# Kernel tuning notes

Hardware: AMD Instinct MI355X
Metric: run time of the kernel (lower is better)

The kernel has to match this reference:

```python
import jax, jax.numpy as jnp
import numpy as np

B, L, E = 128, 512, 128
NUM_Q, NUM_C, DIFF = 10000, 300, 100


def _lin(k, fan_in, fan_out):
    kw, kb = jax.random.split(k)
    s = 1.0 / np.sqrt(fan_in)
    W = jax.random.uniform(kw, (fan_in, fan_out), jnp.float32, -s, s)
    b = jax.random.uniform(kb, (fan_out,), jnp.float32, -s, s)
    return W, b


def setup_inputs() -> dict:
    key = jax.random.key(0)
    ks = jax.random.split(key, 24)
    inp = {
        "q": jax.random.randint(ks[0], (B, L), 0, NUM_Q),
        "c": jax.random.randint(ks[1], (B, L), 0, NUM_C),
        "sd": jax.random.randint(ks[2], (B, L), 0, DIFF + 99),
        "qd": jax.random.randint(ks[3], (B, L), 0, DIFF + 99),
        "a": jax.random.randint(ks[4], (B, L), 0, 2 * NUM_Q + 1),
        "qshft": jax.random.randint(ks[5], (B, L), 0, NUM_Q),
        "cshft": jax.random.randint(ks[6], (B, L), 0, NUM_C),
        "sdshft": jax.random.randint(ks[7], (B, L), 0, DIFF + 99),
        "qdshft": jax.random.randint(ks[8], (B, L), 0, DIFF + 99),
        "knowledge": jax.random.normal(ks[9], (1, E), jnp.float32) * 0.1,
        "q_tab": jax.random.normal(ks[10], (NUM_Q + 1, E), jnp.float32),
        "c_tab": jax.random.normal(ks[11], (NUM_C + 1, E), jnp.float32),
        "sd_tab": jax.random.normal(ks[12], (DIFF + 100, E), jnp.float32),
        "qd_tab": jax.random.normal(ks[13], (DIFF + 100, E), jnp.float32),
        "a_tab": jax.random.normal(ks[14], (2 * NUM_Q + 2, E), jnp.float32),
    }
    for name, fan_in, ki in [("1", 4 * E, 15), ("2", E, 16), ("3", E, 17),
                             ("4", 2 * E, 18), ("5", 2 * E, 19), ("6", 4 * E, 20)]:
        W, b = _lin(ks[ki], fan_in, E)
        inp[f"W{name}"], inp[f"b{name}"] = W, b
    Wf, bf = _lin(ks[21], E, 10)
    inp["Wf"], inp["bf"] = Wf, bf
    return inp


def reference(q, c, sd, qd, a, qshft, cshft, sdshft, qdshft,
              knowledge, q_tab, c_tab, sd_tab, qd_tab, a_tab,
              W1, b1, W2, b2, W3, b3, W4, b4, W5, b5, W6, b6, Wf, bf):
    # Embedding lookups  [B, L, E]
    q_e, c_e = q_tab[q], c_tab[c]
    sd_e, qd_e = sd_tab[sd], qd_tab[qd]
    a_e = a_tab[a]
    # input_data = linear_1(cat(q,c,sd,qd))  [B, L, E]
    inp = jnp.concatenate([q_e, c_e, sd_e, qd_e], -1) @ W1 + b1
    # (target_data in the torch code is dead: never used for the output)

    k0 = jnp.broadcast_to(knowledge, (q.shape[0], knowledge.shape[1]))  # [B, E]

    def step(k, xs):
        x, sd1, a1, qd1 = xs  # each [B, E]
        qq = x - k
        SDFt = jax.nn.sigmoid(qq @ W2 + b2) * jnp.tanh(qq @ W3 + b3)  # dropout=eval
        xa = jnp.concatenate([SDFt, a1], -1)
        PKAt = jax.nn.sigmoid(xa @ W4 + b4) * jnp.tanh(xa @ W5 + b5)
        ins = jnp.concatenate([k, a1, sd1, qd1], -1)
        gK = jax.nn.sigmoid(ins @ W6 + b6)
        k_new = gK * k + (1.0 - gK) * PKAt
        return k_new, k_new @ Wf + bf

    xs = (jnp.swapaxes(inp, 0, 1), jnp.swapaxes(sd_e, 0, 1),
          jnp.swapaxes(a_e, 0, 1), jnp.swapaxes(qd_e, 0, 1))  # [L, B, E]
    _, logits = jax.lax.scan(step, k0, xs)  # [L, B, 10]
    return jax.nn.sigmoid(jnp.swapaxes(logits, 0, 1))  # [B, L, 10]
```

## Files before the change

kernel.cpp:

```cpp
#include <hip/hip_runtime.h>
#include <hip/hip_bf16.h>
#include <stdint.h>

#define E_DIM 128
#define L_SEQ 512
#define B_SZ  128

typedef _Float16 h2 __attribute__((ext_vector_type(2)));

constexpr size_t SZ_W12 = 512 * 128 * 4;
constexpr size_t SZ_TQ  = 10001 * 128 * 4;
constexpr size_t SZ_TC  = 301 * 128 * 4;
constexpr size_t SZ_TS  = 200 * 128 * 4;
constexpr size_t SZ_TA  = 20002 * 128 * 4;
constexpr size_t SZ_K   = (size_t)B_SZ * L_SEQ * 128 * 4;

constexpr size_t OFF_W12  = 0;
constexpr size_t OFF_W13  = OFF_W12 + SZ_W12;
constexpr size_t OFF_BV2  = OFF_W13 + SZ_W12;
constexpr size_t OFF_BV3  = OFF_BV2 + 512;
constexpr size_t OFF_TQ2  = OFF_BV3 + 512;
constexpr size_t OFF_TQ3  = OFF_TQ2 + SZ_TQ;
constexpr size_t OFF_TC2  = OFF_TQ3 + SZ_TQ;
constexpr size_t OFF_TC3  = OFF_TC2 + SZ_TC;
constexpr size_t OFF_TSD2 = OFF_TC3 + SZ_TC;
constexpr size_t OFF_TSD3 = OFF_TSD2 + SZ_TS;
constexpr size_t OFF_TSD6 = OFF_TSD3 + SZ_TS;
constexpr size_t OFF_TQD2 = OFF_TSD6 + SZ_TS;
constexpr size_t OFF_TQD3 = OFF_TQD2 + SZ_TS;
constexpr size_t OFF_TQD6 = OFF_TQD3 + SZ_TS;
constexpr size_t OFF_TA4  = OFF_TQD6 + SZ_TS;
constexpr size_t OFF_TA5  = OFF_TA4 + SZ_TA;
constexpr size_t OFF_TA6  = OFF_TA5 + SZ_TA;
constexpr size_t OFF_K    = OFF_TA6 + SZ_TA;

__device__ __forceinline__ float fdot2f(unsigned int a, unsigned int b, float c) {
#if __has_builtin(__builtin_amdgcn_fdot2)
  return __builtin_amdgcn_fdot2(__builtin_bit_cast(h2, a), __builtin_bit_cast(h2, b), c, false);
#else
  h2 x = __builtin_bit_cast(h2, a), y = __builtin_bit_cast(h2, b);
  return c + (float)x[0] * (float)y[0] + (float)x[1] * (float)y[1];
#endif
}

__device__ __forceinline__ unsigned int packh2(float a, float b) {
  h2 v; v[0] = (_Float16)a; v[1] = (_Float16)b;
  return __builtin_bit_cast(unsigned int, v);
}

__device__ __forceinline__ float fsig(float x) {
  float t = __builtin_amdgcn_exp2f(-1.4426950408889634f * x);
  return __builtin_amdgcn_rcpf(1.0f + t);
}
__device__ __forceinline__ float ftanh(float x) {
  float t = __builtin_amdgcn_exp2f(2.8853900817779268f * x);
  return 1.0f - 2.0f * __builtin_amdgcn_rcpf(t + 1.0f);
}

#define BARRIER_RAW() asm volatile("s_waitcnt lgkmcnt(0)\n\ts_barrier" ::: "memory")

__global__ __launch_bounds__(128, 1) void prepA_kernel(
    const float* __restrict__ W1, const float* __restrict__ W2, const float* __restrict__ W3,
    const float* __restrict__ b1, const float* __restrict__ b2, const float* __restrict__ b3,
    char* __restrict__ ws) {
  float* W12 = (float*)(ws + OFF_W12);
  float* W13 = (float*)(ws + OFF_W13);
  float* bv2 = (float*)(ws + OFF_BV2);
  float* bv3 = (float*)(ws + OFF_BV3);
  __shared__ __align__(16) float rowb[8][128];
  const int j = threadIdx.x;
  const int blk = blockIdx.x;
  if (blk < 8) {
    const float* M = (blk < 4) ? W2 : W3;
    float* dst = (blk < 4) ? W12 : W13;
    const int r0 = (blk & 3) * 128;
    float Mcol[128];
#pragma unroll
    for (int t = 0; t < 128; t++) Mcol[t] = M[t * 128 + j];
    for (int rb = 0; rb < 128; rb += 8) {
#pragma unroll
      for (int rr = 0; rr < 8; rr++) rowb[rr][j] = W1[(r0 + rb + rr) * 128 + j];
      __syncthreads();
#pragma unroll
      for (int rr = 0; rr < 8; rr++) {
        float acc = 0.0f;
        const float4* r4 = (const float4*)rowb[rr];
#pragma unroll
        for (int t4 = 0; t4 < 32; t4++) {
          float4 v = r4[t4];
          acc += v.x * Mcol[4 * t4 + 0];
          acc += v.y * Mcol[4 * t4 + 1];
          acc += v.z * Mcol[4 * t4 + 2];
          acc += v.w * Mcol[4 * t4 + 3];
        }
        dst[(r0 + rb + rr) * 128 + j] = acc;
      }
      __syncthreads();
    }
  } else {
    rowb[0][j] = b1[j];
    __syncthreads();
    float a2 = b2[j], a3 = b3[j];
    for (int t = 0; t < 128; t++) {
      float bb = rowb[0][t];
      a2 += bb * W2[t * 128 + j];
      a3 += bb * W3[t * 128 + j];
    }
    bv2[j] = a2;
    bv3[j] = a3;
  }
}

__global__ __launch_bounds__(128, 1) void prepB_kernel(
    const float* __restrict__ q_tab, const float* __restrict__ c_tab,
    const float* __restrict__ sd_tab, const float* __restrict__ qd_tab,
    const float* __restrict__ a_tab,
    const float* __restrict__ W4, const float* __restrict__ W5, const float* __restrict__ W6,
    const float* __restrict__ b4, const float* __restrict__ b5, const float* __restrict__ b6,
    char* __restrict__ ws) {
  const float* W12 = (const float*)(ws + OFF_W12);
  const float* W13 = (const float*)(ws + OFF_W13);
  const float* bv2 = (const float*)(ws + OFF_BV2);
  const float* bv3 = (const float*)(ws + OFF_BV3);

  const float* src = nullptr; const float* M = nullptr; const float* bias = nullptr;
  float* dst = nullptr; int rows = 0;
  switch (blockIdx.y) {
    case 0:  src = q_tab;  rows = 10001; M = W12;             bias = bv2; dst = (float*)(ws + OFF_TQ2);  break;
    case 1:  src = q_tab;  rows = 10001; M = W13;             bias = bv3; dst = (float*)(ws + OFF_TQ3);  break;
    case 2:  src = c_tab;  rows = 301;   M = W12 + 128 * 128; bias = nullptr; dst = (float*)(ws + OFF_TC2);  break;
    case 3:  src = c_tab;  rows = 301;   M = W13 + 128 * 128; bias = nullptr; dst = (float*)(ws + OFF_TC3);  break;
    case 4:  src = sd_tab; rows = 200;   M = W12 + 256 * 128; bias = nullptr; dst = (float*)(ws + OFF_TSD2); break;
    case 5:  src = sd_tab; rows = 200;   M = W13 + 256 * 128; bias = nullptr; dst = (float*)(ws + OFF_TSD3); break;
    case 6:  src = sd_tab; rows = 200;   M = W6  + 256 * 128; bias = nullptr; dst = (float*)(ws + OFF_TSD6); break;
    case 7:  src = qd_tab; rows = 200;   M = W12 + 384 * 128; bias = nullptr; dst = (float*)(ws + OFF_TQD2); break;
    case 8:  src = qd_tab; rows = 200;   M = W13 + 384 * 128; bias = nullptr; dst = (float*)(ws + OFF_TQD3); break;
    case 9:  src = qd_tab; rows = 200;   M = W6  + 384 * 128; bias = nullptr; dst = (float*)(ws + OFF_TQD6); break;
    case 10: src = a_tab;  rows = 20002; M = W4  + 128 * 128; bias = b4;  dst = (float*)(ws + OFF_TA4);  break;
    case 11: src = a_tab;  rows = 20002; M = W5  + 128 * 128; bias = b5;  dst = (float*)(ws + OFF_TA5);  break;
    default: src = a_tab;  rows = 20002; M = W6  + 128 * 128; bias = b6;  dst = (float*)(ws + OFF_TA6);  break;
  }
  const int row0 = blockIdx.x * 128;
  if (row0 >= rows) return;
  const int j = threadIdx.x;
  float Mcol[128];
#pragma unroll
  for (int t = 0; t < 128; t++) Mcol[t] = M[t * 128 + j];
  const float bj = bias ? bias[j] : 0.0f;
  __shared__ __align__(16) float rowb[8][128];
  const int rend = (row0 + 128 < rows) ? (row0 + 128) : rows;
  for (int rb = row0; rb < rend; rb += 8) {
    const int nr = (rb + 8 <= rend) ? 8 : (rend - rb);
#pragma unroll
    for (int rr = 0; rr < 8; rr++)
      rowb[rr][j] = src[(rb + (rr < nr ? rr : 0)) * 128 + j];
    __syncthreads();
#pragma unroll
    for (int rr = 0; rr < 8; rr++) {
      if (rr < nr) {
        float acc = bj;
        const float4* r4 = (const float4*)rowb[rr];
#pragma unroll
        for (int t4 = 0; t4 < 32; t4++) {
          float4 v = r4[t4];
          acc += v.x * Mcol[4 * t4 + 0];
          acc += v.y * Mcol[4 * t4 + 1];
          acc += v.z * Mcol[4 * t4 + 2];
          acc += v.w * Mcol[4 * t4 + 3];
        }
        dst[(rb + rr) * 128 + j] = acc;
      }
    }
    __syncthreads();
  }
}


#define PREFETCH(S, P) do {                                                   \
    int _s = (S);                                                             \
    int _qi = idxb[0][_s], _ci = idxb[1][_s], _si = idxb[2][_s];              \
    int _di = idxb[3][_s], _ai = idxb[4][_s];                                 \
    P##q2 = Tq2[_qi * 128 + j]; P##q3 = Tq3[_qi * 128 + j];                   \
    P##c2 = Tc2[_ci * 128 + j]; P##c3 = Tc3[_ci * 128 + j];                   \
    P##s2 = Ts2[_si * 128 + j]; P##s3 = Ts3[_si * 128 + j];                   \
    P##s6 = Ts6[_si * 128 + j];                                               \
    P##d2 = Td2[_di * 128 + j]; P##d3 = Td3[_di * 128 + j];                   \
    P##d6 = Td6[_di * 128 + j];                                               \
    P##a4 = Ta4[_ai * 128 + j]; P##a5 = Ta5[_ai * 128 + j];                   \
    P##a6 = Ta6[_ai * 128 + j];                                               \
  } while (0)

#define SCAN_STEP(P, S2, L) do {                                              \
                                           \
    float u2a = 0.f, u2b = 0.f, u3a = 0.f, u3b = 0.f, u6a = 0.f, u6b = 0.f;   \
    {                                                                         \
      const uint4* kp4 = ((const uint4*)kpair) + 8 * h;                       \
      _Pragma("unroll")                                                       \
      for (int i = 0; i < 8; i++) {                                           \
        uint4 kv = kp4[i];                                                    \
        u2a = fdot2f(kv.x, w2h[4 * i + 0], u2a);                              \
        u3a = fdot2f(kv.x, w3h[4 * i + 0], u3a);                              \
        u6a = fdot2f(kv.x, w6h[4 * i + 0], u6a);                              \
        u2b = fdot2f(kv.y, w2h[4 * i + 1], u2b);                              \
        u3b = fdot2f(kv.y, w3h[4 * i + 1], u3b);                              \
        u6b = fdot2f(kv.y, w6h[4 * i + 1], u6b);                              \
        u2a = fdot2f(kv.z, w2h[4 * i + 2], u2a);                              \
        u3a = fdot2f(kv.z, w3h[4 * i + 2], u3a);                              \
        u6a = fdot2f(kv.z, w6h[4 * i + 2], u6a);                              \
        u2b = fdot2f(kv.w, w2h[4 * i + 3], u2b);                              \
        u3b = fdot2f(kv.w, w3h[4 * i + 3], u3b);                              \
        u6b = fdot2f(kv.w, w6h[4 * i + 3], u6b);                              \
      }                                                                       \
    }                                                                         \
    pA[0][tid] = u2a + u2b; pA[1][tid] = u3a + u3b; pA[2][tid] = u6a + u6b;   \
    BARRIER_RAW();                                                    \
    float o2 = pA[0][tid ^ 128], o3 = pA[1][tid ^ 128], o6 = pA[2][tid ^ 128];\
    float U2 = (P##q2 + P##c2 + P##s2 + P##d2) - (u2a + u2b + o2);            \
    float U3 = (P##q3 + P##c3 + P##s3 + P##d3) - (u3a + u3b + o3);            \
    float U6 = (P##a6 + P##s6 + P##d6) + (u6a + u6b + o6);                    \
    float sdft = fsig(U2) * ftanh(U3);                                        \
    float g = fsig(U6);                                                       \
    if (!h) ((_Float16*)sdfp)[j] = (_Float16)sdft;                            \
    BARRIER_RAW();                                                    \
                                           \
    float u4a = 0.f, u4b = 0.f, u5a = 0.f, u5b = 0.f;                         \
    {                                                                         \
      const uint4* sp4 = ((const uint4*)sdfp) + 8 * h;                        \
      _Pragma("unroll")                                                       \
      for (int i = 0; i < 8; i++) {                                           \
        uint4 sv = sp4[i];                                                    \
        u4a = fdot2f(sv.x, w4h[4 * i + 0], u4a);                              \
        u5a = fdot2f(sv.x, w5h[4 * i + 0], u5a);                              \
        u4b = fdot2f(sv.y, w4h[4 * i + 1], u4b);                              \
        u5b = fdot2f(sv.y, w5h[4 * i + 1], u5b);                              \
        u4a = fdot2f(sv.z, w4h[4 * i + 2], u4a);                              \
        u5a = fdot2f(sv.z, w5h[4 * i + 2], u5a);                              \
        u4b = fdot2f(sv.w, w4h[4 * i + 3], u4b);                              \
        u5b = fdot2f(sv.w, w5h[4 * i + 3], u5b);                              \
      }                                                                       \
    }                                                                         \
    pB[0][tid] = u4a + u4b; pB[1][tid] = u5a + u5b;                           \
    BARRIER_RAW();                                                    \
    float o4 = pB[0][tid ^ 128], o5 = pB[1][tid ^ 128];                       \
    float pk = fsig(u4a + u4b + o4 + P##a4) * ftanh(u5a + u5b + o5 + P##a5);  \
    k = g * k + (1.0f - g) * pk;                                              \
    if (h) ((_Float16*)kpair)[j] = (_Float16)k;                               \
    BARRIER_RAW();                                                    \
    if (!h) Kout[((size_t)(base + (L))) * 128 + j] = k;                       \
    PREFETCH(S2, P);                                                          \
  } while (0)

__global__ __launch_bounds__(256, 1) void scan_kernel(
    const int* __restrict__ q, const int* __restrict__ c, const int* __restrict__ sd,
    const int* __restrict__ qd, const int* __restrict__ a,
    const float* __restrict__ knowledge,
    const float* __restrict__ W2, const float* __restrict__ W3, const float* __restrict__ W4,
    const float* __restrict__ W5, const float* __restrict__ W6,
    char* __restrict__ ws) {
  const int tid = threadIdx.x;
  const int j = tid & 127;
  const int h = tid >> 7;
  const int b = blockIdx.x;
  const int base = b * L_SEQ;

  const float* Tq2 = (const float*)(ws + OFF_TQ2);
  const float* Tq3 = (const float*)(ws + OFF_TQ3);
  const float* Tc2 = (const float*)(ws + OFF_TC2);
  const float* Tc3 = (const float*)(ws + OFF_TC3);
  const float* Ts2 = (const float*)(ws + OFF_TSD2);
  const float* Ts3 = (const float*)(ws + OFF_TSD3);
  const float* Ts6 = (const float*)(ws + OFF_TSD6);
  const float* Td2 = (const float*)(ws + OFF_TQD2);
  const float* Td3 = (const float*)(ws + OFF_TQD3);
  const float* Td6 = (const float*)(ws + OFF_TQD6);
  const float* Ta4 = (const float*)(ws + OFF_TA4);
  const float* Ta5 = (const float*)(ws + OFF_TA5);
  const float* Ta6 = (const float*)(ws + OFF_TA6);
  float* Kout = (float*)(ws + OFF_K);

  __shared__ int idxb[5][L_SEQ];
  __shared__ __align__(16) unsigned int kpair[64];
  __shared__ __align__(16) unsigned int sdfp[64];
  __shared__ float pA[3][256];
  __shared__ float pB[2][256];

  idxb[0][tid] = q[base + tid];  idxb[0][tid + 256] = q[base + tid + 256];
  idxb[1][tid] = c[base + tid];  idxb[1][tid + 256] = c[base + tid + 256];
  idxb[2][tid] = sd[base + tid]; idxb[2][tid + 256] = sd[base + tid + 256];
  idxb[3][tid] = qd[base + tid]; idxb[3][tid + 256] = qd[base + tid + 256];
  idxb[4][tid] = a[base + tid];  idxb[4][tid + 256] = a[base + tid + 256];

  unsigned int w2h[32], w3h[32], w6h[32], w4h[32], w5h[32];
  const int t0 = h * 64;
#pragma unroll
  for (int p = 0; p < 32; p++) {
    w2h[p] = packh2(W2[(t0 + 2 * p) * 128 + j], W2[(t0 + 2 * p + 1) * 128 + j]);
    w3h[p] = packh2(W3[(t0 + 2 * p) * 128 + j], W3[(t0 + 2 * p + 1) * 128 + j]);
    w6h[p] = packh2(W6[(t0 + 2 * p) * 128 + j], W6[(t0 + 2 * p + 1) * 128 + j]);
    w4h[p] = packh2(W4[(t0 + 2 * p) * 128 + j], W4[(t0 + 2 * p + 1) * 128 + j]);
    w5h[p] = packh2(W5[(t0 + 2 * p) * 128 + j], W5[(t0 + 2 * p + 1) * 128 + j]);
  }

  float k = knowledge[j];
  if (h) ((_Float16*)kpair)[j] = (_Float16)k;
  __syncthreads();

  float gAq2, gAq3, gAc2, gAc3, gAs2, gAs3, gAs6, gAd2, gAd3, gAd6, gAa4, gAa5, gAa6;
  float gBq2, gBq3, gBc2, gBc3, gBs2, gBs3, gBs6, gBd2, gBd3, gBd6, gBa4, gBa5, gBa6;
  PREFETCH(0, gA);
  PREFETCH(1, gB);

#pragma unroll 1
  for (int m = 0; m < L_SEQ / 2; m++) {
    const int l0 = 2 * m;
    const int s2 = (l0 + 2 < L_SEQ) ? (l0 + 2) : (L_SEQ - 1);
    const int s3 = (l0 + 3 < L_SEQ) ? (l0 + 3) : (L_SEQ - 1);
    SCAN_STEP(gA, s2, l0);
    SCAN_STEP(gB, s3, l0 + 1);
  }
}

__global__ __launch_bounds__(256, 4) void logits_kernel(
    const float* __restrict__ Wf, const float* __restrict__ bf,
    const char* __restrict__ ws, float* __restrict__ out) {
  const float* K = (const float*)(ws + OFF_K);
  const int t = blockIdx.x * 256 + threadIdx.x;
  if (t >= B_SZ * L_SEQ * 10) return;
  const int r = t / 10;
  const int i = t - 10 * r;
  float acc = bf[i];
  const float* kr = K + (size_t)r * 128;
#pragma unroll 8
  for (int jj = 0; jj < 128; jj++) acc += kr[jj] * Wf[jj * 10 + i];
  out[t] = fsig(acc);
}

extern "C" void kernel_launch(void* const* d_in, const int* in_sizes, int n_in,
                              void* d_out, int out_size, void* d_ws, size_t ws_size,
                              hipStream_t stream) {
  const int* q  = (const int*)d_in[0];
  const int* c  = (const int*)d_in[1];
  const int* sd = (const int*)d_in[2];
  const int* qd = (const int*)d_in[3];
  const int* a  = (const int*)d_in[4];
  const float* knowledge = (const float*)d_in[9];
  const float* q_tab  = (const float*)d_in[10];
  const float* c_tab  = (const float*)d_in[11];
  const float* sd_tab = (const float*)d_in[12];
  const float* qd_tab = (const float*)d_in[13];
  const float* a_tab  = (const float*)d_in[14];
  const float* W1 = (const float*)d_in[15];
  const float* b1 = (const float*)d_in[16];
  const float* W2 = (const float*)d_in[17];
  const float* b2 = (const float*)d_in[18];
  const float* W3 = (const float*)d_in[19];
  const float* b3 = (const float*)d_in[20];
  const float* W4 = (const float*)d_in[21];
  const float* b4 = (const float*)d_in[22];
  const float* W5 = (const float*)d_in[23];
  const float* b5 = (const float*)d_in[24];
  const float* W6 = (const float*)d_in[25];
  const float* b6 = (const float*)d_in[26];
  const float* Wf = (const float*)d_in[27];
  const float* bf = (const float*)d_in[28];
  char* ws = (char*)d_ws;
  float* out = (float*)d_out;

  prepA_kernel<<<9, 128, 0, stream>>>(W1, W2, W3, b1, b2, b3, ws);
  prepB_kernel<<<dim3(157, 13), 128, 0, stream>>>(q_tab, c_tab, sd_tab, qd_tab, a_tab,
                                                  W4, W5, W6, b4, b5, b6, ws);
  scan_kernel<<<B_SZ, 256, 0, stream>>>(q, c, sd, qd, a, knowledge, W2, W3, W4, W5, W6, ws);
  logits_kernel<<<(B_SZ * L_SEQ * 10 + 255) / 256, 256, 0, stream>>>(Wf, bf, ws, out);
}
```

Before: 924.5 us.

## Use MFMA for table pre-projection, shuffle-based scan reduction, row-wise logits

Replaces the scalar FP32 table-projection kernel with two fp16 MFMA GEMM kernels that project each embedding table through several weight slices at once. The scan kernel is remapped so that the two half-dot-product partners sit in the same wavefront, which turns two LDS exchange barriers per step into lane shuffles, and one barrier moves after the prefetch. The logits kernel now computes all 10 outputs per row from shared-memory weights using float4 loads. This lowers prep and scan overhead but rounds the precomputed tables to fp16 inputs, so accuracy may suffer.

```diff
diff --git a/kernel.cpp b/kernel.cpp
--- a/kernel.cpp
+++ b/kernel.cpp
@@ -7,13 +7,14 @@
 #define B_SZ  128
 
 typedef _Float16 h2 __attribute__((ext_vector_type(2)));
+typedef _Float16 f16x8 __attribute__((ext_vector_type(8)));
+typedef float f32x4 __attribute__((ext_vector_type(4)));
 
 constexpr size_t SZ_W12 = 512 * 128 * 4;
 constexpr size_t SZ_TQ  = 10001 * 128 * 4;
 constexpr size_t SZ_TC  = 301 * 128 * 4;
 constexpr size_t SZ_TS  = 200 * 128 * 4;
 constexpr size_t SZ_TA  = 20002 * 128 * 4;
-constexpr size_t SZ_K   = (size_t)B_SZ * L_SEQ * 128 * 4;
 
 constexpr size_t OFF_W12  = 0;
 constexpr size_t OFF_W13  = OFF_W12 + SZ_W12;
@@ -111,65 +112,136 @@
   }
 }
 
-__global__ __launch_bounds__(128, 1) void prepB_kernel(
+template <int NSEG>
+__global__ __launch_bounds__(256, 1) void gemm_tabs_kernel(
     const float* __restrict__ q_tab, const float* __restrict__ c_tab,
     const float* __restrict__ sd_tab, const float* __restrict__ qd_tab,
     const float* __restrict__ a_tab,
     const float* __restrict__ W4, const float* __restrict__ W5, const float* __restrict__ W6,
     const float* __restrict__ b4, const float* __restrict__ b5, const float* __restrict__ b6,
     char* __restrict__ ws) {
+  constexpr int WD  = NSEG * 128;
+  constexpr int SPAN = WD / 4;
+  constexpr int NCT = SPAN / 16;
+
+  __shared__ _Float16 BT[WD][136];
+  __shared__ _Float16 At[32][136];
+  __shared__ float biasL[384];
+
   const float* W12 = (const float*)(ws + OFF_W12);
   const float* W13 = (const float*)(ws + OFF_W13);
   const float* bv2 = (const float*)(ws + OFF_BV2);
   const float* bv3 = (const float*)(ws + OFF_BV3);
 
-  const float* src = nullptr; const float* M = nullptr; const float* bias = nullptr;
-  float* dst = nullptr; int rows = 0;
-  switch (blockIdx.y) {
-    case 0:  src = q_tab;  rows = 10001; M = W12;             bias = bv2; dst = (float*)(ws + OFF_TQ2);  break;
-    case 1:  src = q_tab;  rows = 10001; M = W13;             bias = bv3; dst = (float*)(ws + OFF_TQ3);  break;
-    case 2:  src = c_tab;  rows = 301;   M = W12 + 128 * 128; bias = nullptr; dst = (float*)(ws + OFF_TC2);  break;
-    case 3:  src = c_tab;  rows = 301;   M = W13 + 128 * 128; bias = nullptr; dst = (float*)(ws + OFF_TC3);  break;
-    case 4:  src = sd_tab; rows = 200;   M = W12 + 256 * 128; bias = nullptr; dst = (float*)(ws + OFF_TSD2); break;
-    case 5:  src = sd_tab; rows = 200;   M = W13 + 256 * 128; bias = nullptr; dst = (float*)(ws + OFF_TSD3); break;
-    case 6:  src = sd_tab; rows = 200;   M = W6  + 256 * 128; bias = nullptr; dst = (float*)(ws + OFF_TSD6); break;
-    case 7:  src = qd_tab; rows = 200;   M = W12 + 384 * 128; bias = nullptr; dst = (float*)(ws + OFF_TQD2); break;
-    case 8:  src = qd_tab; rows = 200;   M = W13 + 384 * 128; bias = nullptr; dst = (float*)(ws + OFF_TQD3); break;
-    case 9:  src = qd_tab; rows = 200;   M = W6  + 384 * 128; bias = nullptr; dst = (float*)(ws + OFF_TQD6); break;
-    case 10: src = a_tab;  rows = 20002; M = W4  + 128 * 128; bias = b4;  dst = (float*)(ws + OFF_TA4);  break;
-    case 11: src = a_tab;  rows = 20002; M = W5  + 128 * 128; bias = b5;  dst = (float*)(ws + OFF_TA5);  break;
-    default: src = a_tab;  rows = 20002; M = W6  + 128 * 128; bias = b6;  dst = (float*)(ws + OFF_TA6);  break;
-  }
-  const int row0 = blockIdx.x * 128;
-  if (row0 >= rows) return;
-  const int j = threadIdx.x;
-  float Mcol[128];
-#pragma unroll
-  for (int t = 0; t < 128; t++) Mcol[t] = M[t * 128 + j];
-  const float bj = bias ? bias[j] : 0.0f;
-  __shared__ __align__(16) float rowb[8][128];
-  const int rend = (row0 + 128 < rows) ? (row0 + 128) : rows;
-  for (int rb = row0; rb < rend; rb += 8) {
-    const int nr = (rb + 8 <= rend) ? 8 : (rend - rb);
-#pragma unroll
-    for (int rr = 0; rr < 8; rr++)
-      rowb[rr][j] = src[(rb + (rr < nr ? rr : 0)) * 128 + j];
+  const int bid = blockIdx.x;
+  const int tid = threadIdx.x;
+  const int wv = tid >> 6, ln = tid & 63;
+
+  const float* src; int rows; int blk_in;
+  const float* bsrc[3]; int koff[3]; const float* bias[3]; float* dst[3];
+  if (NSEG == 2) {
+    if (bid < 79) { src = q_tab; rows = 10001; blk_in = bid;
+      bsrc[0] = W12; bsrc[1] = W13; koff[0] = koff[1] = 0;
+      bias[0] = bv2; bias[1] = bv3;
+      dst[0] = (float*)(ws + OFF_TQ2); dst[1] = (float*)(ws + OFF_TQ3);
+    } else { src = c_tab; rows = 301; blk_in = bid - 79;
+      bsrc[0] = W12; bsrc[1] = W13; koff[0] = koff[1] = 128;
+      bias[0] = bias[1] = nullptr;
+      dst[0] = (float*)(ws + OFF_TC2); dst[1] = (float*)(ws + OFF_TC3);
+    }
+    bsrc[2] = nullptr; koff[2] = 0; bias[2] = nullptr; dst[2] = nullptr;
+  } else {
+    if (bid < 2) { src = sd_tab; rows = 200; blk_in = bid;
+      bsrc[0] = W12; bsrc[1] = W13; bsrc[2] = W6; koff[0] = koff[1] = koff[2] = 256;
+      bias[0] = bias[1] = bias[2] = nullptr;
+      dst[0] = (float*)(ws + OFF_TSD2); dst[1] = (float*)(ws + OFF_TSD3); dst[2] = (float*)(ws + OFF_TSD6);
+    } else if (bid < 4) { src = qd_tab; rows = 200; blk_in = bid - 2;
+      bsrc[0] = W12; bsrc[1] = W13; bsrc[2] = W6; koff[0] = koff[1] = koff[2] = 384;
+      bias[0] = bias[1] = bias[2] = nullptr;
+      dst[0] = (float*)(ws + OFF_TQD2); dst[1] = (float*)(ws + OFF_TQD3); dst[2] = (float*)(ws + OFF_TQD6);
+    } else { src = a_tab; rows = 20002; blk_in = bid - 4;
+      bsrc[0] = W4; bsrc[1] = W5; bsrc[2] = W6; koff[0] = koff[1] = koff[2] = 128;
+      bias[0] = b4; bias[1] = b5; bias[2] = b6;
+      dst[0] = (float*)(ws + OFF_TA4); dst[1] = (float*)(ws + OFF_TA5); dst[2] = (float*)(ws + OFF_TA6);
+    }
+  }
+
+#pragma unroll
+  for (int s = 0; s < NSEG; s++) {
+    const float* M = bsrc[s] + (size_t)koff[s] * 128;
+    const int jj = tid & 127, kb = tid >> 7;
+    for (int k0 = 0; k0 < 128; k0 += 2) {
+      const int k = k0 + kb;
+      BT[s * 128 + jj][k] = (_Float16)M[k * 128 + jj];
+    }
+    if (tid < 128) biasL[s * 128 + tid] = bias[s] ? bias[s][tid] : 0.0f;
+  }
+  __syncthreads();
+
+  f16x8 bf[NCT][4];
+#pragma unroll
+  for (int ct = 0; ct < NCT; ct++)
+#pragma unroll
+    for (int kt = 0; kt < 4; kt++) {
+      const int col = wv * SPAN + ct * 16 + (ln & 15);
+      const int k = kt * 32 + (ln >> 4) * 8;
+      bf[ct][kt] = *(const f16x8*)&BT[col][k];
+    }
+  float bvl[NCT];
+#pragma unroll
+  for (int ct = 0; ct < NCT; ct++) bvl[ct] = biasL[wv * SPAN + ct * 16 + (ln & 15)];
+
+  const int row_base = blk_in * 128;
+  for (int ch = 0; ch < 4; ch++) {
+    const int row0 = row_base + ch * 32;
+    {
+      const int r = tid >> 3, cb = (tid & 7) * 16;
+      int sr = row0 + r; if (sr >= rows) sr = rows - 1;
+      const float4* s4 = (const float4*)(src + (size_t)sr * 128 + cb);
+      float4 v0 = s4[0], v1 = s4[1], v2 = s4[2], v3 = s4[3];
+      f16x8 lo, hi;
+      lo[0] = (_Float16)v0.x; lo[1] = (_Float16)v0.y; lo[2] = (_Float16)v0.z; lo[3] = (_Float16)v0.w;
+      lo[4] = (_Float16)v1.x; lo[5] = (_Float16)v1.y; lo[6] = (_Float16)v1.z; lo[7] = (_Float16)v1.w;
+      hi[0] = (_Float16)v2.x; hi[1] = (_Float16)v2.y; hi[2] = (_Float16)v2.z; hi[3] = (_Float16)v2.w;
+      hi[4] = (_Float16)v3.x; hi[5] = (_Float16)v3.y; hi[6] = (_Float16)v3.z; hi[7] = (_Float16)v3.w;
+      *(f16x8*)&At[r][cb] = lo;
+      *(f16x8*)&At[r][cb + 8] = hi;
+    }
     __syncthreads();
-#pragma unroll
-    for (int rr = 0; rr < 8; rr++) {
-      if (rr < nr) {
-        float acc = bj;
-        const float4* r4 = (const float4*)rowb[rr];
-#pragma unroll
-        for (int t4 = 0; t4 < 32; t4++) {
-          float4 v = r4[t4];
-          acc += v.x * Mcol[4 * t4 + 0];
-          acc += v.y * Mcol[4 * t4 + 1];
-          acc += v.z * Mcol[4 * t4 + 2];
-          acc += v.w * Mcol[4 * t4 + 3];
+    f16x8 af[2][4];
+#pragma unroll
+    for (int rt = 0; rt < 2; rt++)
+#pragma unroll
+      for (int kt = 0; kt < 4; kt++) {
+        const int row = rt * 16 + (ln & 15);
+        const int k = kt * 32 + (ln >> 4) * 8;
+        af[rt][kt] = *(const f16x8*)&At[row][k];
+      }
+    f32x4 acc[2][NCT];
+#pragma unroll
+    for (int rt = 0; rt < 2; rt++)
+#pragma unroll
+      for (int ct = 0; ct < NCT; ct++) acc[rt][ct] = (f32x4){0.f, 0.f, 0.f, 0.f};
+#pragma unroll
+    for (int kt = 0; kt < 4; kt++)
+#pragma unroll
+      for (int ct = 0; ct < NCT; ct++)
+#pragma unroll
+        for (int rt = 0; rt < 2; rt++)
+          acc[rt][ct] = __builtin_amdgcn_mfma_f32_16x16x32_f16(af[rt][kt], bf[ct][kt], acc[rt][ct], 0, 0, 0);
+#pragma unroll
+    for (int ct = 0; ct < NCT; ct++) {
+      const int gcol = wv * SPAN + ct * 16 + (ln & 15);
+      const int seg = gcol >> 7, col = gcol & 127;
+      float* D = dst[seg];
+      const float bv = bvl[ct];
+#pragma unroll
+      for (int rt = 0; rt < 2; rt++)
+#pragma unroll
+        for (int e = 0; e < 4; e++) {
+          const int row = row0 + rt * 16 + (ln >> 4) * 4 + e;
+          if (row < rows) D[(size_t)row * 128 + col] = acc[rt][ct][e] + bv;
         }
-        dst[(rb + rr) * 128 + j] = acc;
-      }
     }
     __syncthreads();
   }
@@ -191,7 +263,6 @@
   } while (0)
 
 #define SCAN_STEP(P, S2, L) do {                                              \
-                                           \
     float u2a = 0.f, u2b = 0.f, u3a = 0.f, u3b = 0.f, u6a = 0.f, u6b = 0.f;   \
     {                                                                         \
       const uint4* kp4 = ((const uint4*)kpair) + 8 * h;                       \
@@ -212,17 +283,17 @@
         u6b = fdot2f(kv.w, w6h[4 * i + 3], u6b);                              \
       }                                                                       \
     }                                                                         \
-    pA[0][tid] = u2a + u2b; pA[1][tid] = u3a + u3b; pA[2][tid] = u6a + u6b;   \
-    BARRIER_RAW();                                                    \
-    float o2 = pA[0][tid ^ 128], o3 = pA[1][tid ^ 128], o6 = pA[2][tid ^ 128];\
-    float U2 = (P##q2 + P##c2 + P##s2 + P##d2) - (u2a + u2b + o2);            \
-    float U3 = (P##q3 + P##c3 + P##s3 + P##d3) - (u3a + u3b + o3);            \
-    float U6 = (P##a6 + P##s6 + P##d6) + (u6a + u6b + o6);                    \
+    float U2p = u2a + u2b, U3p = u3a + u3b, U6p = u6a + u6b;                  \
+    U2p += __shfl_xor(U2p, 32);                                               \
+    U3p += __shfl_xor(U3p, 32);                                               \
+    U6p += __shfl_xor(U6p, 32);                                               \
+    float U2 = (P##q2 + P##c2 + P##s2 + P##d2) - U2p;                         \
+    float U3 = (P##q3 + P##c3 + P##s3 + P##d3) - U3p;                         \
+    float U6 = (P##a6 + P##s6 + P##d6) + U6p;                                 \
     float sdft = fsig(U2) * ftanh(U3);                                        \
     float g = fsig(U6);                                                       \
     if (!h) ((_Float16*)sdfp)[j] = (_Float16)sdft;                            \
-    BARRIER_RAW();                                                    \
-                                           \
+    BARRIER_RAW();                                    \
     float u4a = 0.f, u4b = 0.f, u5a = 0.f, u5b = 0.f;                         \
     {                                                                         \
       const uint4* sp4 = ((const uint4*)sdfp) + 8 * h;                        \
@@ -239,15 +310,15 @@
         u5b = fdot2f(sv.w, w5h[4 * i + 3], u5b);                              \
       }                                                                       \
     }                                                                         \
-    pB[0][tid] = u4a + u4b; pB[1][tid] = u5a + u5b;                           \
-    BARRIER_RAW();                                                    \
-    float o4 = pB[0][tid ^ 128], o5 = pB[1][tid ^ 128];                       \
-    float pk = fsig(u4a + u4b + o4 + P##a4) * ftanh(u5a + u5b + o5 + P##a5);  \
+    float U4p = u4a + u4b, U5p = u5a + u5b;                                   \
+    U4p += __shfl_xor(U4p, 32);                                               \
+    U5p += __shfl_xor(U5p, 32);                                               \
+    float pk = fsig(U4p + P##a4) * ftanh(U5p + P##a5);                        \
     k = g * k + (1.0f - g) * pk;                                              \
     if (h) ((_Float16*)kpair)[j] = (_Float16)k;                               \
-    BARRIER_RAW();                                                    \
     if (!h) Kout[((size_t)(base + (L))) * 128 + j] = k;                       \
     PREFETCH(S2, P);                                                          \
+    BARRIER_RAW();                                       \
   } while (0)
 
 __global__ __launch_bounds__(256, 1) void scan_kernel(
@@ -258,8 +329,9 @@
     const float* __restrict__ W5, const float* __restrict__ W6,
     char* __restrict__ ws) {
   const int tid = threadIdx.x;
-  const int j = tid & 127;
-  const int h = tid >> 7;
+  const int wv = tid >> 6, ln = tid & 63;
+  const int j = (wv << 5) | (ln & 31);
+  const int h = ln >> 5;
   const int b = blockIdx.x;
   const int base = b * L_SEQ;
 
@@ -281,8 +353,6 @@
   __shared__ int idxb[5][L_SEQ];
   __shared__ __align__(16) unsigned int kpair[64];
   __shared__ __align__(16) unsigned int sdfp[64];
-  __shared__ float pA[3][256];
-  __shared__ float pB[2][256];
 
   idxb[0][tid] = q[base + tid];  idxb[0][tid + 256] = q[base + tid + 256];
   idxb[1][tid] = c[base + tid];  idxb[1][tid + 256] = c[base + tid + 256];
@@ -320,19 +390,34 @@
   }
 }
 
-__global__ __launch_bounds__(256, 4) void logits_kernel(
+__global__ __launch_bounds__(256, 2) void logits_kernel(
     const float* __restrict__ Wf, const float* __restrict__ bf,
     const char* __restrict__ ws, float* __restrict__ out) {
+  __shared__ float WfL[1280];
+  __shared__ float bfL[10];
+  const int tid = threadIdx.x;
+  for (int i = tid; i < 1280; i += 256) WfL[i] = Wf[i];
+  if (tid < 10) bfL[tid] = bf[tid];
+  __syncthreads();
   const float* K = (const float*)(ws + OFF_K);
-  const int t = blockIdx.x * 256 + threadIdx.x;
-  if (t >= B_SZ * L_SEQ * 10) return;
-  const int r = t / 10;
-  const int i = t - 10 * r;
-  float acc = bf[i];
-  const float* kr = K + (size_t)r * 128;
-#pragma unroll 8
-  for (int jj = 0; jj < 128; jj++) acc += kr[jj] * Wf[jj * 10 + i];
-  out[t] = fsig(acc);
+  const int nrows = B_SZ * L_SEQ;
+  for (int r = blockIdx.x * 256 + tid; r < nrows; r += gridDim.x * 256) {
+    const float4* kr = (const float4*)(K + (size_t)r * 128);
+    float acc[10];
+#pragma unroll
+    for (int i = 0; i < 10; i++) acc[i] = bfL[i];
+#pragma unroll
+    for (int t4 = 0; t4 < 32; t4++) {
+      float4 v = kr[t4];
+#pragma unroll
+      for (int i = 0; i < 10; i++)
+        acc[i] += v.x * WfL[(4 * t4 + 0) * 10 + i] + v.y * WfL[(4 * t4 + 1) * 10 + i] +
+                  v.z * WfL[(4 * t4 + 2) * 10 + i] + v.w * WfL[(4 * t4 + 3) * 10 + i];
+    }
+    float* o = out + (size_t)r * 10;
+#pragma unroll
+    for (int i = 0; i < 10; i++) o[i] = fsig(acc[i]);
+  }
 }
 
 extern "C" void kernel_launch(void* const* d_in, const int* in_sizes, int n_in,
@@ -367,8 +452,10 @@
   float* out = (float*)d_out;
 
   prepA_kernel<<<9, 128, 0, stream>>>(W1, W2, W3, b1, b2, b3, ws);
-  prepB_kernel<<<dim3(157, 13), 128, 0, stream>>>(q_tab, c_tab, sd_tab, qd_tab, a_tab,
-                                                  W4, W5, W6, b4, b5, b6, ws);
+  gemm_tabs_kernel<2><<<82, 256, 0, stream>>>(q_tab, c_tab, sd_tab, qd_tab, a_tab,
+                                              W4, W5, W6, b4, b5, b6, ws);
+  gemm_tabs_kernel<3><<<161, 256, 0, stream>>>(q_tab, c_tab, sd_tab, qd_tab, a_tab,
+                                               W4, W5, W6, b4, b5, b6, ws);
   scan_kernel<<<B_SZ, 256, 0, stream>>>(q, c, sd, qd, a, knowledge, W2, W3, W4, W5, W6, ws);
-  logits_kernel<<<(B_SZ * L_SEQ * 10 + 255) / 256, 256, 0, stream>>>(Wf, bf, ws, out);
-}
+  logits_kernel<<<256, 256, 0, stream>>>(Wf, bf, ws, out);
+}
```

Measured after the change: 793.8 us. 14.1% less time.
